# Optimization experiments

Hardware: AMD Instinct MI355X
Metric: run time of the kernel (lower is better)

Reference implementation:

```python
import jax, jax.numpy as jnp
import numpy as np

B, N, C, H = 8, 1025, 1024, 16


def setup_inputs() -> dict:
    key = jax.random.key(0)
    k1, k2, k3, k4 = jax.random.split(key, 4)
    x = jax.random.normal(k1, (B, N, C), dtype=jnp.float32)
    w_qkv = jax.random.normal(k2, (3 * C, C), dtype=jnp.float32) * (C ** -0.5)
    w_proj = jax.random.normal(k3, (C, C), dtype=jnp.float32) * (C ** -0.5)
    b_proj = jax.random.normal(k4, (C,), dtype=jnp.float32) * 0.01
    return {"x": x, "w_qkv": w_qkv, "w_proj": w_proj, "b_proj": b_proj}


def reference(x, w_qkv, w_proj, b_proj):
    b, n, c = x.shape
    hd = c // H
    scale = hd ** -0.5
    qkv = (x @ w_qkv.T).reshape(b, n, 3, H, hd).transpose(2, 0, 3, 1, 4)
    q, k, v = qkv[0], qkv[1], qkv[2]
    # standard QK attention path
    attn_ori = jax.nn.softmax(jnp.einsum('bhnd,bhmd->bhnm', q, k) * scale, axis=-1)
    # CLIP-Surgery V-V self-correlation path (settings='' -> same scale)
    attn_vv = jax.nn.softmax(jnp.einsum('bhnd,bhmd->bhnm', v, v) * scale, axis=-1)
    x_ori = jnp.einsum('bhnm,bhmd->bhnd', attn_ori, v).transpose(0, 2, 1, 3).reshape(b, n, c)
    x_new = jnp.einsum('bhnm,bhmd->bhnd', attn_vv, v).transpose(0, 2, 1, 3).reshape(b, n, c)
    out_vv = x_new @ w_proj.T + b_proj
    out_ori = x_ori @ w_proj.T + b_proj
    return (out_vv, out_ori)
```

## Files before the change

kernel.cpp:

```cpp
#include <hip/hip_runtime.h>

typedef unsigned short ushort_t;
typedef __attribute__((ext_vector_type(8))) __bf16 bf16x8;
typedef __attribute__((ext_vector_type(4))) float f32x4;

constexpr int B_ = 8, N_ = 1025, C_ = 1024, H_ = 16, HD = 64;
constexpr int M_QKV = B_ * N_;
constexpr int M_PROJ = 2 * B_ * N_;
constexpr int K_ = 1024;
constexpr int NT = 1032;
constexpr size_t S1 = (size_t)B_ * H_ * N_ * HD;
constexpr size_t VT_SZ = (size_t)B_ * H_ * HD * NT;

__device__ __forceinline__ ushort_t f2bf(float f) {
    union { float f; unsigned u; } a; a.f = f;
    unsigned r = a.u + 0x7FFFu + ((a.u >> 16) & 1u);
    return (ushort_t)(r >> 16);
}
__device__ __forceinline__ ushort_t f2bf_fast(float f) {
    return (ushort_t)((__float_as_uint(f) + 0x8000u) >> 16);
}
__device__ __forceinline__ unsigned pk2(float x, float y) {
    unsigned a = __float_as_uint(x) + 0x8000u;
    unsigned b = __float_as_uint(y) + 0x8000u;
    return (a >> 16) | (b & 0xffff0000u);
}
__device__ __forceinline__ uint4 pack8(float4 x, float4 y) {
    return make_uint4(pk2(x.x, x.y), pk2(x.z, x.w), pk2(y.x, y.y), pk2(y.z, y.w));
}

union U4 { uint4 v; ushort_t s[8]; };

__device__ __forceinline__ void gload16(const ushort_t* g, ushort_t* l) {
    __builtin_amdgcn_global_load_lds(
        (const __attribute__((address_space(1))) void*)g,
        (__attribute__((address_space(3))) void*)l, 16, 0, 0);
}

__global__ __launch_bounds__(256)
void conv_bf16(const float* __restrict__ src, ushort_t* __restrict__ dst, int n8) {
    const int i = blockIdx.x * 256 + threadIdx.x;
    if (i < n8) {
        const float4* s = (const float4*)src + 2 * (size_t)i;
        ((uint4*)dst)[i] = pack8(s[0], s[1]);
    }
}

__global__ __launch_bounds__(256)
void gemm_qkv(const ushort_t* __restrict__ A, const ushort_t* __restrict__ Bm,
              ushort_t* __restrict__ q, ushort_t* __restrict__ k,
              ushort_t* __restrict__ v, ushort_t* __restrict__ vT) {
    __shared__ ushort_t As[128 * 32];
    __shared__ ushort_t Bs[128 * 32];
    const int tid = threadIdx.x;
    const int wave = tid >> 6, lane = tid & 63;
    const int quad = lane >> 4, l16 = lane & 15;
    const int m0 = blockIdx.y * 128, n0 = blockIdx.x * 128;
    const int wm = (wave & 1) * 64, wn = (wave >> 1) * 64;

    const int col8 = (tid & 3) * 8;
    const int row0 = tid >> 2;
    const int ar0 = min(m0 + row0,      M_QKV - 1);
    const int ar1 = min(m0 + row0 + 64, M_QKV - 1);
    const ushort_t* ga0 = A + (size_t)ar0 * K_ + col8;
    const ushort_t* ga1 = A + (size_t)ar1 * K_ + col8;
    const ushort_t* gb0 = Bm + (size_t)(n0 + row0) * K_ + col8;
    const ushort_t* gb1 = Bm + (size_t)(n0 + row0 + 64) * K_ + col8;
    ushort_t* lA0 = As + tid * 8;
    ushort_t* lA1 = As + (tid + 256) * 8;
    ushort_t* lB0 = Bs + tid * 8;
    ushort_t* lB1 = Bs + (tid + 256) * 8;

    f32x4 acc[4][4] = {};

    for (int k0 = 0; k0 < K_; k0 += 32) {
        __syncthreads();
        gload16(ga0 + k0, lA0);
        gload16(ga1 + k0, lA1);
        gload16(gb0 + k0, lB0);
        gload16(gb1 + k0, lB1);
        __syncthreads();
        bf16x8 af[4], bfr[4];
#pragma unroll
        for (int i = 0; i < 4; i++) {
            af[i]  = *(const bf16x8*)(As + (wm + i * 16 + l16) * 32 + quad * 8);
            bfr[i] = *(const bf16x8*)(Bs + (wn + i * 16 + l16) * 32 + quad * 8);
        }
#pragma unroll
        for (int im = 0; im < 4; im++)
#pragma unroll
            for (int in = 0; in < 4; in++)
                acc[im][in] = __builtin_amdgcn_mfma_f32_16x16x32_bf16(af[im], bfr[in], acc[im][in], 0, 0, 0);
    }

#pragma unroll
    for (int im = 0; im < 4; im++) {
#pragma unroll
        for (int in = 0; in < 4; in++) {
            const int gcol = n0 + wn + in * 16 + l16;
            const int which = gcol >> 10;
            const int c = gcol & 1023;
            const int h = c >> 6, d = c & 63;
            ushort_t* dst = which == 0 ? q : (which == 1 ? k : v);
            const float sc = (which == 0) ? 0.125f : 1.0f;
#pragma unroll
            for (int r = 0; r < 4; r++) {
                const int grow = m0 + wm + im * 16 + quad * 4 + r;
                if (grow < M_QKV) {
                    const int b = grow / N_;
                    const int nn = grow - b * N_;
                    const ushort_t val = f2bf(acc[im][in][r] * sc);
                    const size_t bh = (size_t)(b * H_ + h);
                    dst[(bh * N_ + nn) * HD + d] = val;
                    if (which == 2)
                        vT[(bh * HD + d) * NT + nn] = val;
                }
            }
        }
    }
}

__global__ __launch_bounds__(512, 4)
void attn_kernel(const ushort_t* __restrict__ q, const ushort_t* __restrict__ k,
                 const ushort_t* __restrict__ v, const ushort_t* __restrict__ vT,
                 ushort_t* __restrict__ xvv, ushort_t* __restrict__ xori) {
    __shared__ ushort_t Kd[2][64 * 64];
    __shared__ ushort_t Vd[2][64 * 64];
    __shared__ ushort_t Td[2][64 * 64];
    __shared__ ushort_t Ps[128][64];

    const int tid = threadIdx.x;
    const int wave = tid >> 6, lane = tid & 63;
    const int quad = lane >> 4, l16 = lane & 15;
    const int bh = blockIdx.y;
    const int b = bh >> 4, h = bh & 15;

    const size_t base  = (size_t)bh * N_ * HD;
    const size_t baseT = (size_t)bh * HD * NT;
    const int qstart = min((int)blockIdx.x * 128, N_ - 128);
    const int qr0 = qstart + wave * 16;

    const int swz   = (l16 & 7) << 3;
    const int pswz  = (l16 >> 3) << 4;
    const int pwxor = (quad >> 1) << 4;

    const int srow = tid >> 3;
    const int scol = 8 * ((tid & 7) ^ (srow & 7));
    const int ld = tid * 8;

    bf16x8 qq[2], qv[2];
    {
        const int qrow = qr0 + l16;
#pragma unroll
        for (int kk = 0; kk < 2; kk++) {
            U4 uq, uv;
            uq.v = *(const uint4*)(q + base + (size_t)qrow * HD + kk * 32 + quad * 8);
            uv.v = *(const uint4*)(v + base + (size_t)qrow * HD + kk * 32 + quad * 8);
            qq[kk] = *(const bf16x8*)uq.s;
            qv[kk] = *(const bf16x8*)uv.s;
        }
    }

    float l0a[4] = {0.f, 0.f, 0.f, 0.f}, l1a[4] = {0.f, 0.f, 0.f, 0.f};
    f32x4 o0[4] = {}, o1[4] = {};

    const int nkt = (N_ + 63) / 64;

    gload16(k + base + (size_t)srow * HD + scol,   &Kd[0][ld]);
    gload16(v + base + (size_t)srow * HD + scol,   &Vd[0][ld]);
    gload16(vT + baseT + (size_t)srow * NT + scol, &Td[0][ld]);

    for (int kt = 0; kt < nkt; kt++) {
        const int key0 = kt * 64;
        const bool tail = (key0 + 64 > N_);
        const int cur = kt & 1;

        __syncthreads();

        if (kt + 1 < nkt) {
            const int kn = key0 + 64;
            const int nb = cur ^ 1;
            const int kk0 = min(kn + srow, N_ - 1);
            gload16(k + base + (size_t)kk0 * HD + scol, &Kd[nb][ld]);
            gload16(v + base + (size_t)kk0 * HD + scol, &Vd[nb][ld]);
            gload16(vT + baseT + (size_t)srow * NT + kn + scol, &Td[nb][ld]);
        }

        const ushort_t* Kc = Kd[cur];
        const ushort_t* Vc = Vd[cur];
        const ushort_t* Tc = Td[cur];

        f32x4 s[4];
        __builtin_amdgcn_s_setprio(1);
#pragma unroll
        for (int t = 0; t < 4; t++) {
            const int row = (t * 16 + l16) * 64;
            bf16x8 b0 = *(const bf16x8*)(Kc + row + ((quad * 8) ^ swz));
            bf16x8 b1 = *(const bf16x8*)(Kc + row + ((32 + quad * 8) ^ swz));
            f32x4 a = {};
            a = __builtin_amdgcn_mfma_f32_16x16x32_bf16(qq[0], b0, a, 0, 0, 0);
            a = __builtin_amdgcn_mfma_f32_16x16x32_bf16(qq[1], b1, a, 0, 0, 0);
            s[t] = a;
        }
        __builtin_amdgcn_s_setprio(0);

        if (tail) {
#pragma unroll
            for (int t = 0; t < 4; t++)
                if (key0 + t * 16 + l16 >= N_) {
#pragma unroll
                    for (int r = 0; r < 4; r++) s[t][r] = -1e30f;
                }
        }
#pragma unroll
        for (int t = 0; t < 4; t++)
#pragma unroll
            for (int r = 0; r < 4; r++) {
                const float p = __expf(s[t][r]);
                l0a[r] += p;
                Ps[wave * 16 + quad * 4 + r][(t * 16 + l16) ^ pwxor] = f2bf_fast(p);
            }
        {
            bf16x8 pa0 = *(const bf16x8*)(&Ps[wave * 16 + l16][(quad * 8) ^ pswz]);
            bf16x8 pa1 = *(const bf16x8*)(&Ps[wave * 16 + l16][(32 + quad * 8) ^ pswz]);
            __builtin_amdgcn_s_setprio(1);
#pragma unroll
            for (int t = 0; t < 4; t++) {
                const int row = (t * 16 + l16) * 64;
                bf16x8 bv0 = *(const bf16x8*)(Tc + row + ((quad * 8) ^ swz));
                bf16x8 bv1 = *(const bf16x8*)(Tc + row + ((32 + quad * 8) ^ swz));
                o0[t] = __builtin_amdgcn_mfma_f32_16x16x32_bf16(pa0, bv0, o0[t], 0, 0, 0);
                o0[t] = __builtin_amdgcn_mfma_f32_16x16x32_bf16(pa1, bv1, o0[t], 0, 0, 0);
            }
            __builtin_amdgcn_s_setprio(0);
        }

        __builtin_amdgcn_s_setprio(1);
#pragma unroll
        for (int t = 0; t < 4; t++) {
            const int row = (t * 16 + l16) * 64;
            bf16x8 b0 = *(const bf16x8*)(Vc + row + ((quad * 8) ^ swz));
            bf16x8 b1 = *(const bf16x8*)(Vc + row + ((32 + quad * 8) ^ swz));
            f32x4 a = {};
            a = __builtin_amdgcn_mfma_f32_16x16x32_bf16(qv[0], b0, a, 0, 0, 0);
            a = __builtin_amdgcn_mfma_f32_16x16x32_bf16(qv[1], b1, a, 0, 0, 0);
            s[t] = a;
        }
        __builtin_amdgcn_s_setprio(0);
        if (tail) {
#pragma unroll
            for (int t = 0; t < 4; t++)
                if (key0 + t * 16 + l16 >= N_) {
#pragma unroll
                    for (int r = 0; r < 4; r++) s[t][r] = -1e30f;
                }
        }
#pragma unroll
        for (int t = 0; t < 4; t++)
#pragma unroll
            for (int r = 0; r < 4; r++) {
                const float p = __expf(s[t][r] * 0.125f);
                l1a[r] += p;
                Ps[wave * 16 + quad * 4 + r][(t * 16 + l16) ^ pwxor] = f2bf_fast(p);
            }
        {
            bf16x8 pa0 = *(const bf16x8*)(&Ps[wave * 16 + l16][(quad * 8) ^ pswz]);
            bf16x8 pa1 = *(const bf16x8*)(&Ps[wave * 16 + l16][(32 + quad * 8) ^ pswz]);
            __builtin_amdgcn_s_setprio(1);
#pragma unroll
            for (int t = 0; t < 4; t++) {
                const int row = (t * 16 + l16) * 64;
                bf16x8 bv0 = *(const bf16x8*)(Tc + row + ((quad * 8) ^ swz));
                bf16x8 bv1 = *(const bf16x8*)(Tc + row + ((32 + quad * 8) ^ swz));
                o1[t] = __builtin_amdgcn_mfma_f32_16x16x32_bf16(pa0, bv0, o1[t], 0, 0, 0);
                o1[t] = __builtin_amdgcn_mfma_f32_16x16x32_bf16(pa1, bv1, o1[t], 0, 0, 0);
            }
            __builtin_amdgcn_s_setprio(0);
        }
    }

#pragma unroll
    for (int r = 0; r < 4; r++) {
        float L0 = l0a[r], L1 = l1a[r];
#pragma unroll
        for (int off = 1; off < 16; off <<= 1) {
            L0 += __shfl_xor(L0, off);
            L1 += __shfl_xor(L1, off);
        }
        const int row = qr0 + quad * 4 + r;
        const float inv0 = 1.0f / L0;
        const float inv1 = 1.0f / L1;
        const size_t rb = (size_t)(b * N_ + row) * C_ + h * HD;
#pragma unroll
        for (int t = 0; t < 4; t++) {
            const int d = t * 16 + l16;
            xori[rb + d] = f2bf(o0[t][r] * inv0);
            xvv[rb + d]  = f2bf(o1[t][r] * inv1);
        }
    }
}

__global__ __launch_bounds__(256)
void gemm_proj(const ushort_t* __restrict__ A, const ushort_t* __restrict__ Bm,
               const float* __restrict__ bias, float* __restrict__ out) {
    __shared__ ushort_t As[128 * 32];
    __shared__ ushort_t Bs[128 * 32];
    const int tid = threadIdx.x;
    const int wave = tid >> 6, lane = tid & 63;
    const int quad = lane >> 4, l16 = lane & 15;
    const int m0 = blockIdx.y * 128, n0 = blockIdx.x * 128;
    const int wm = (wave & 1) * 64, wn = (wave >> 1) * 64;

    const int col8 = (tid & 3) * 8;
    const int row0 = tid >> 2;
    const int ar0 = min(m0 + row0,      M_PROJ - 1);
    const int ar1 = min(m0 + row0 + 64, M_PROJ - 1);
    const ushort_t* ga0 = A + (size_t)ar0 * K_ + col8;
    const ushort_t* ga1 = A + (size_t)ar1 * K_ + col8;
    const ushort_t* gb0 = Bm + (size_t)(n0 + row0) * K_ + col8;
    const ushort_t* gb1 = Bm + (size_t)(n0 + row0 + 64) * K_ + col8;
    ushort_t* lA0 = As + tid * 8;
    ushort_t* lA1 = As + (tid + 256) * 8;
    ushort_t* lB0 = Bs + tid * 8;
    ushort_t* lB1 = Bs + (tid + 256) * 8;

    f32x4 acc[4][4] = {};

    for (int k0 = 0; k0 < K_; k0 += 32) {
        __syncthreads();
        gload16(ga0 + k0, lA0);
        gload16(ga1 + k0, lA1);
        gload16(gb0 + k0, lB0);
        gload16(gb1 + k0, lB1);
        __syncthreads();
        bf16x8 af[4], bfr[4];
#pragma unroll
        for (int i = 0; i < 4; i++) {
            af[i]  = *(const bf16x8*)(As + (wm + i * 16 + l16) * 32 + quad * 8);
            bfr[i] = *(const bf16x8*)(Bs + (wn + i * 16 + l16) * 32 + quad * 8);
        }
#pragma unroll
        for (int im = 0; im < 4; im++)
#pragma unroll
            for (int in = 0; in < 4; in++)
                acc[im][in] = __builtin_amdgcn_mfma_f32_16x16x32_bf16(af[im], bfr[in], acc[im][in], 0, 0, 0);
    }

#pragma unroll
    for (int im = 0; im < 4; im++) {
#pragma unroll
        for (int in = 0; in < 4; in++) {
            const int gcol = n0 + wn + in * 16 + l16;
            const float bb = bias[gcol];
#pragma unroll
            for (int r = 0; r < 4; r++) {
                const int grow = m0 + wm + im * 16 + quad * 4 + r;
                if (grow < M_PROJ)
                    out[(size_t)grow * C_ + gcol] = acc[im][in][r] + bb;
            }
        }
    }
}

extern "C" void kernel_launch(void* const* d_in, const int* in_sizes, int n_in,
                              void* d_out, int out_size, void* d_ws, size_t ws_size,
                              hipStream_t stream) {
    const float* x      = (const float*)d_in[0];
    const float* w_qkv  = (const float*)d_in[1];
    const float* w_proj = (const float*)d_in[2];
    const float* b_proj = (const float*)d_in[3];
    float* out = (float*)d_out;

    ushort_t* ws = (ushort_t*)d_ws;
    ushort_t* x_bf     = ws;
    ushort_t* xvv      = ws;
    ushort_t* xori     = ws + S1;
    ushort_t* v        = ws + 2 * S1;
    ushort_t* wproj_bf = ws + 2 * S1;

    ushort_t* q        = (ushort_t*)d_out;
    ushort_t* k        = (ushort_t*)d_out + S1;
    ushort_t* vT       = (ushort_t*)d_out + 2 * S1;
    ushort_t* wqkv_bf  = (ushort_t*)d_out + 2 * S1 + VT_SZ;

    {
        const int n8x = (int)(S1 / 8);
        conv_bf16<<<(n8x + 255) / 256, 256, 0, stream>>>(x, x_bf, n8x);
        const int n8w = 3 * C_ * C_ / 8;
        conv_bf16<<<(n8w + 255) / 256, 256, 0, stream>>>(w_qkv, wqkv_bf, n8w);
    }
    {
        dim3 grid(3072 / 128, (M_QKV + 127) / 128);
        gemm_qkv<<<grid, 256, 0, stream>>>(x_bf, wqkv_bf, q, k, v, vT);
    }
    {
        dim3 grid((N_ + 127) / 128, B_ * H_);
        attn_kernel<<<grid, 512, 0, stream>>>(q, k, v, vT, xvv, xori);
    }
    {
        const int n8p = C_ * C_ / 8;
        conv_bf16<<<(n8p + 255) / 256, 256, 0, stream>>>(w_proj, wproj_bf, n8p);
    }
    {
        dim3 grid(1024 / 128, (M_PROJ + 127) / 128);
        gemm_proj<<<grid, 256, 0, stream>>>(xvv, wproj_bf, b_proj, out);
    }
}
```

Before: 400.5 us.

## Use exp2 softmax, remap attention blocks for L2 locality, hoist V^T LDS loads

Folds log2(e) into the Q scaling and the V-V scale so the softmax uses exp2f instead of __expf. The attention grid is flattened and remapped so that 8 consecutive blocks cover different heads in the same query-tile group, aiming for better L2/XCD locality. V^T fragments are loaded from LDS once per key tile and reused by both PV products instead of being read twice. Ps is padded to 72 columns, which adds LDS and changes the bank mapping alongside the existing XOR swizzle, and holding the hoisted fragments raises register pressure.

```diff
diff --git a/kernel.cpp b/kernel.cpp
--- a/kernel.cpp
+++ b/kernel.cpp
@@ -102,7 +102,7 @@
             const int c = gcol & 1023;
             const int h = c >> 6, d = c & 63;
             ushort_t* dst = which == 0 ? q : (which == 1 ? k : v);
-            const float sc = (which == 0) ? 0.125f : 1.0f;
+            const float sc = (which == 0) ? 0.18033688f : 1.0f;
 #pragma unroll
             for (int r = 0; r < 4; r++) {
                 const int grow = m0 + wm + im * 16 + quad * 4 + r;
@@ -127,17 +127,23 @@
     __shared__ ushort_t Kd[2][64 * 64];
     __shared__ ushort_t Vd[2][64 * 64];
     __shared__ ushort_t Td[2][64 * 64];
-    __shared__ ushort_t Ps[128][64];
+    __shared__ ushort_t Ps[128][72];
 
     const int tid = threadIdx.x;
     const int wave = tid >> 6, lane = tid & 63;
     const int quad = lane >> 4, l16 = lane & 15;
-    const int bh = blockIdx.y;
+
+    const int lin = blockIdx.x;
+    const int r8 = lin & 7;
+    const int j = lin >> 3;
+    const int g = j / 9;
+    const int qt = j - g * 9;
+    const int bh = g * 8 + r8;
     const int b = bh >> 4, h = bh & 15;
 
     const size_t base  = (size_t)bh * N_ * HD;
     const size_t baseT = (size_t)bh * HD * NT;
-    const int qstart = min((int)blockIdx.x * 128, N_ - 128);
+    const int qstart = min(qt * 128, N_ - 128);
     const int qr0 = qstart + wave * 16;
 
     const int swz   = (l16 & 7) << 3;
@@ -189,6 +195,14 @@
         const ushort_t* Kc = Kd[cur];
         const ushort_t* Vc = Vd[cur];
         const ushort_t* Tc = Td[cur];
+
+        bf16x8 tva[4], tvb[4];
+#pragma unroll
+        for (int t = 0; t < 4; t++) {
+            const int row = (t * 16 + l16) * 64;
+            tva[t] = *(const bf16x8*)(Tc + row + ((quad * 8) ^ swz));
+            tvb[t] = *(const bf16x8*)(Tc + row + ((32 + quad * 8) ^ swz));
+        }
 
         f32x4 s[4];
         __builtin_amdgcn_s_setprio(1);
@@ -216,7 +230,7 @@
         for (int t = 0; t < 4; t++)
 #pragma unroll
             for (int r = 0; r < 4; r++) {
-                const float p = __expf(s[t][r]);
+                const float p = exp2f(s[t][r]);
                 l0a[r] += p;
                 Ps[wave * 16 + quad * 4 + r][(t * 16 + l16) ^ pwxor] = f2bf_fast(p);
             }
@@ -226,11 +240,8 @@
             __builtin_amdgcn_s_setprio(1);
 #pragma unroll
             for (int t = 0; t < 4; t++) {
-                const int row = (t * 16 + l16) * 64;
-                bf16x8 bv0 = *(const bf16x8*)(Tc + row + ((quad * 8) ^ swz));
-                bf16x8 bv1 = *(const bf16x8*)(Tc + row + ((32 + quad * 8) ^ swz));
-                o0[t] = __builtin_amdgcn_mfma_f32_16x16x32_bf16(pa0, bv0, o0[t], 0, 0, 0);
-                o0[t] = __builtin_amdgcn_mfma_f32_16x16x32_bf16(pa1, bv1, o0[t], 0, 0, 0);
+                o0[t] = __builtin_amdgcn_mfma_f32_16x16x32_bf16(pa0, tva[t], o0[t], 0, 0, 0);
+                o0[t] = __builtin_amdgcn_mfma_f32_16x16x32_bf16(pa1, tvb[t], o0[t], 0, 0, 0);
             }
             __builtin_amdgcn_s_setprio(0);
         }
@@ -259,7 +270,7 @@
         for (int t = 0; t < 4; t++)
 #pragma unroll
             for (int r = 0; r < 4; r++) {
-                const float p = __expf(s[t][r] * 0.125f);
+                const float p = exp2f(s[t][r] * 0.18033688f);
                 l1a[r] += p;
                 Ps[wave * 16 + quad * 4 + r][(t * 16 + l16) ^ pwxor] = f2bf_fast(p);
             }
@@ -269,11 +280,8 @@
             __builtin_amdgcn_s_setprio(1);
 #pragma unroll
             for (int t = 0; t < 4; t++) {
-                const int row = (t * 16 + l16) * 64;
-                bf16x8 bv0 = *(const bf16x8*)(Tc + row + ((quad * 8) ^ swz));
-                bf16x8 bv1 = *(const bf16x8*)(Tc + row + ((32 + quad * 8) ^ swz));
-                o1[t] = __builtin_amdgcn_mfma_f32_16x16x32_bf16(pa0, bv0, o1[t], 0, 0, 0);
-                o1[t] = __builtin_amdgcn_mfma_f32_16x16x32_bf16(pa1, bv1, o1[t], 0, 0, 0);
+                o1[t] = __builtin_amdgcn_mfma_f32_16x16x32_bf16(pa0, tva[t], o1[t], 0, 0, 0);
+                o1[t] = __builtin_amdgcn_mfma_f32_16x16x32_bf16(pa1, tvb[t], o1[t], 0, 0, 0);
             }
             __builtin_amdgcn_s_setprio(0);
         }
@@ -394,8 +402,7 @@
         gemm_qkv<<<grid, 256, 0, stream>>>(x_bf, wqkv_bf, q, k, v, vT);
     }
     {
-        dim3 grid((N_ + 127) / 128, B_ * H_);
-        attn_kernel<<<grid, 512, 0, stream>>>(q, k, v, vT, xvv, xori);
+        attn_kernel<<<dim3(9 * B_ * H_), 512, 0, stream>>>(q, k, v, vT, xvv, xori);
     }
     {
         const int n8p = C_ * C_ / 8;
```

Result: slower. 426.7 us (+6.5%).
